# Performance work log

Measured on AMD Instinct MI355X. Metric: run time of the kernel, lower is better.

## Reference

```python
import jax, jax.numpy as jnp
import numpy as np

B, C, N, K = 2, 128, 8192, 16
EPS = 1e-5
SLOPE = 0.2


def _knn_idx(coords, k):
    # coords: [B, 3, N] -> idx: [B, N, k] (k nearest neighbors, self excluded)
    pts = jnp.transpose(coords, (0, 2, 1))            # [B, N, 3]
    sq = jnp.sum(pts * pts, axis=-1)                  # [B, N]
    d2 = sq[:, :, None] + sq[:, None, :] - 2.0 * jnp.einsum('bnd,bmd->bnm', pts, pts)
    _, idx = jax.lax.top_k(-d2, k + 1)                # nearest first; first is self (dist 0)
    return idx[:, :, 1:]


def _graph_feature(feats, idx):
    # feats: [B, C, N], idx: [B, N, k] -> [B, 2C, N, k] = concat(center, neighbor - center)
    gather = jax.vmap(lambda f, i: f[:, i])           # [C,N],[N,k] -> [C,N,k]
    neigh = gather(feats, idx)                        # [B, C, N, k]
    center = jnp.broadcast_to(feats[..., None], neigh.shape)
    return jnp.concatenate([center, neigh - center], axis=1)


def _inorm(x):
    # InstanceNorm2d, affine=False: normalize per (b, c) over spatial dims
    m = jnp.mean(x, axis=(2, 3), keepdims=True)
    v = jnp.var(x, axis=(2, 3), keepdims=True)
    return (x - m) * jax.lax.rsqrt(v + EPS)


def _block(x, W):
    # 1x1 conv (no bias) + instance norm + leaky relu
    y = jnp.einsum('oc,bcnk->bonk', W, x)
    return jax.nn.leaky_relu(_inorm(y), SLOPE)


def setup_inputs() -> dict:
    key = jax.random.key(0)
    k0, k1, k2, k3, k4 = jax.random.split(key, 5)
    coords = jax.random.normal(k0, (B, 3, N), dtype=jnp.float32)
    features = jax.random.normal(k1, (B, C, N), dtype=jnp.float32)
    W1 = jax.random.normal(k2, (C, 2 * C), dtype=jnp.float32) * 0.05
    W2 = jax.random.normal(k3, (2 * C, 2 * C), dtype=jnp.float32) * 0.05
    W3 = jax.random.normal(k4, (C, 4 * C), dtype=jnp.float32) * 0.05
    return {"coords": coords, "features": features, "W1": W1, "W2": W2, "W3": W3}


def reference(coords, features, W1, W2, W3):
    idx = _knn_idx(coords, K)                  # same coords for both gathers -> compute once
    x0 = features                              # [B, C, N]
    x1 = _block(_graph_feature(x0, idx), W1).max(axis=-1)   # [B, C, N]
    x2 = _block(_graph_feature(x1, idx), W2).max(axis=-1)   # [B, 2C, N]
    x3 = jnp.concatenate([x0, x1, x2], axis=1)              # [B, 4C, N]
    y = jnp.einsum('oc,bcn->bon', W3, x3)[..., None]        # [B, C, N, 1]
    out = jax.nn.leaky_relu(_inorm(y), SLOPE)[..., 0]       # [B, C, N]
    return out
```

## Files before the change

kernel.cpp:

```cpp
#include <hip/hip_runtime.h>
#include <math.h>

#define NB 2
#define NPTS 8192
#define CH 128
#define KNN 16
#define K17 17
#define EPSI 1e-5f
#define SLOPE 0.2f
#define NCH 32
#define CHSZ 256
#define SCAP 16
#define BIGF 3.0e38f

#define OFF_IDX   0L
#define OFF_X3    1048576L
#define OFF_UV    34603008L
#define OFF_SURV  OFF_X3
#define OFF_YM    68157440L
#define OFF_CNT   OFF_YM
#define OFF_PA    (OFF_YM + 2097152L)
#define OFF_TAU   (OFF_YM + 10485760L)
#define OFF_WM1   84934656L
#define OFF_WM2   85065728L
#define OFF_STATS 85327872L
#define OFF_PTS4  85336064L


__global__ void zero_stats_k(float* __restrict__ stats) {
  int t = blockIdx.x * 256 + threadIdx.x;
  if (t < 2048) stats[t] = 0.f;
}

__global__ void transpose_x0_k(const float* __restrict__ feat, float* __restrict__ x3) {
  __shared__ float tile[32][33];
  int b = blockIdx.z;
  int n0 = blockIdx.x * 32, c0 = blockIdx.y * 32;
  int tx = threadIdx.x;
  for (int ty = threadIdx.y; ty < 32; ty += 8)
    tile[ty][tx] = feat[((long)b * CH + c0 + ty) * NPTS + n0 + tx];
  __syncthreads();
  for (int ty = threadIdx.y; ty < 32; ty += 8)
    x3[((long)b * NPTS + n0 + ty) * 512 + c0 + tx] = tile[tx][ty];
}

__global__ void prep_w_k(const float* __restrict__ W1, const float* __restrict__ W2,
                         float* __restrict__ Wm1, float* __restrict__ Wm2) {
  int t = blockIdx.x * 256 + threadIdx.x;
  if (t < 256 * 128) {
    int r = t >> 7, k = t & 127;
    Wm1[t] = (r < 128) ? (W1[r * 256 + k] - W1[r * 256 + 128 + k])
                       : W1[(r - 128) * 256 + 128 + k];
  }
  if (t < 512 * 128) {
    int r = t >> 7, k = t & 127;
    Wm2[t] = (r < 256) ? (W2[r * 256 + k] - W2[r * 256 + 128 + k])
                       : W2[(r - 256) * 256 + 128 + k];
  }
}

__global__ void knn_prep_k(const float* __restrict__ coords, float4* __restrict__ pts) {
  int b = blockIdx.y;
  int i = blockIdx.x * 256 + threadIdx.x;
  const float* cb = coords + (long)b * 3 * NPTS;
  float x = cb[i], y = cb[NPTS + i], z = cb[2 * NPTS + i];
  float sq = __fadd_rn(__fadd_rn(__fmul_rn(x, x), __fmul_rn(y, y)), __fmul_rn(z, z));
  pts[(long)b * NPTS + i] = make_float4(x, y, z, sq);
}

#define DIST(pi, pj, d2)                                                          \
  float dot = __fadd_rn(__fadd_rn(__fmul_rn((pi).x, (pj).x), __fmul_rn((pi).y, (pj).y)), \
                        __fmul_rn((pi).z, (pj).z));                               \
  float d2 = __fsub_rn(__fadd_rn((pi).w, (pj).w), __fmul_rn(2.0f, dot));

#define KNN_INSERT(d2v, jv)                                              \
  if ((d2v) < d[K17 - 1]) {                                              \
    _Pragma("unroll")                                                    \
    for (int s = K17 - 1; s > 0; --s) {                                  \
      if ((d2v) < d[s - 1]) { d[s] = d[s - 1]; id[s] = id[s - 1]; }      \
      else if ((d2v) < d[s]) { d[s] = (d2v); id[s] = (jv); }             \
    }                                                                    \
    if ((d2v) < d[0]) { d[0] = (d2v); id[0] = (jv); }                    \
  }

__global__ __launch_bounds__(256) void knn_phaseA_k(const float4* __restrict__ pts,
                                                    float2* __restrict__ pa) {
  int b = blockIdx.y;
  int ib = blockIdx.x & 127;
  int sg = blockIdx.x >> 7;
  int i = ib * 64 + (threadIdx.x & 63);
  int sub = sg * 4 + (threadIdx.x >> 6);
  const float4* P = pts + (long)b * NPTS;
  float4 pi = P[i];
  float d0 = BIGF, d1 = BIGF;
  int i0 = 0x7fffffff, i1 = 0x7fffffff;
  int j0 = sub * 64;
  for (int jj = 0; jj < 64; ++jj) {
    float4 pj = P[j0 + jj];
    DIST(pi, pj, d2)
    if (d2 < d1) {
      if (d2 < d0) { d1 = d0; i1 = i0; d0 = d2; i0 = j0 + jj; }
      else { d1 = d2; i1 = j0 + jj; }
    }
  }
  long base = (((long)b * NPTS + i) * 32 + sub) * 2;
  pa[base] = make_float2(d0, __int_as_float(i0));
  pa[base + 1] = make_float2(d1, __int_as_float(i1));
}

__global__ __launch_bounds__(256) void knn_mergeA_k(const float2* __restrict__ pa,
                                                    float* __restrict__ tau) {
  int b = blockIdx.y;
  int i = blockIdx.x * 256 + threadIdx.x;
  float d[K17]; int id[K17];
#pragma unroll
  for (int s = 0; s < K17; ++s) { d[s] = BIGF; id[s] = 0x7fffffff; }
  long base = ((long)b * NPTS + i) * 64;
  for (int c = 0; c < 64; ++c) {
    float2 v = pa[base + c];
    if (v.x < d[K17 - 1]) {
      int j = __float_as_int(v.y);
      KNN_INSERT(v.x, j);
    }
  }
  tau[(long)b * NPTS + i] = d[K17 - 1];
}

__global__ __launch_bounds__(256) void knn_filter_k(const float4* __restrict__ pts,
                                                    const float* __restrict__ tau,
                                                    float2* __restrict__ surv,
                                                    int* __restrict__ counts) {
  int b = blockIdx.z;
  int i = blockIdx.x * 256 + threadIdx.x;
  int chunk = blockIdx.y;
  const float4* P = pts + (long)b * NPTS;
  float4 pi = P[i];
  float t = tau[(long)b * NPTS + i];
  long sbase = (((long)b * NPTS + i) * NCH + chunk) * SCAP;
  int cnt = 0;
  int j0 = chunk * CHSZ;
#pragma unroll 2
  for (int jj = 0; jj < CHSZ; ++jj) {
    float4 pj = P[j0 + jj];
    DIST(pi, pj, d2)
    if (d2 <= t) {
      if (cnt < SCAP) surv[sbase + cnt] = make_float2(d2, __int_as_float(j0 + jj));
      cnt++;
    }
  }
  counts[((long)b * NPTS + i) * NCH + chunk] = cnt;
}

__global__ __launch_bounds__(256) void knn_mergeB_k(const float2* __restrict__ surv,
                                                    const int* __restrict__ counts,
                                                    const float4* __restrict__ pts,
                                                    int* __restrict__ idxo) {
  __shared__ float2 lds[8][K17][32];
  __shared__ int ldbad[8][32];
  int b = blockIdx.y;
  int pl = threadIdx.x & 31;
  int sub = threadIdx.x >> 5;
  int i = blockIdx.x * 32 + pl;
  float d[K17]; int id[K17];
#pragma unroll
  for (int s = 0; s < K17; ++s) { d[s] = BIGF; id[s] = 0x7fffffff; }
  long cbase = ((long)b * NPTS + i) * NCH;
  int bad = 0;
  for (int c = sub * 4; c < sub * 4 + 4; ++c) {
    int cnt = counts[cbase + c];
    if (cnt > SCAP) { bad = 1; cnt = SCAP; }
    long sb = (cbase + c) * SCAP;
    for (int p = 0; p < cnt; ++p) {
      float2 v = surv[sb + p];
      if (v.x < d[K17 - 1]) {
        int j = __float_as_int(v.y);
        KNN_INSERT(v.x, j);
      }
    }
  }
  ldbad[sub][pl] = bad;
#pragma unroll
  for (int s = 0; s < K17; ++s) lds[sub][s][pl] = make_float2(d[s], __int_as_float(id[s]));
  __syncthreads();
  if ((sub & 1) == 0) {
#pragma unroll
    for (int s = 0; s < K17; ++s) {
      float2 v = lds[sub + 1][s][pl];
      if (v.x < d[K17 - 1]) {
        int j = __float_as_int(v.y);
        KNN_INSERT(v.x, j);
      }
    }
  }
  __syncthreads();
  if ((sub & 1) == 0) {
#pragma unroll
    for (int s = 0; s < K17; ++s) lds[sub >> 1][s][pl] = make_float2(d[s], __int_as_float(id[s]));
  }
  __syncthreads();
  if (sub < 2) {
#pragma unroll
    for (int s = 0; s < K17; ++s) {
      float2 v = lds[2 * sub][s][pl];
      d[s] = v.x; id[s] = __float_as_int(v.y);
    }
#pragma unroll
    for (int s = 0; s < K17; ++s) {
      float2 v = lds[2 * sub + 1][s][pl];
      if (v.x < d[K17 - 1]) {
        int j = __float_as_int(v.y);
        KNN_INSERT(v.x, j);
      }
    }
  }
  __syncthreads();
  if (sub < 2) {
#pragma unroll
    for (int s = 0; s < K17; ++s) lds[sub][s][pl] = make_float2(d[s], __int_as_float(id[s]));
  }
  __syncthreads();
  if (sub == 0) {
#pragma unroll
    for (int s = 0; s < K17; ++s) {
      float2 v = lds[0][s][pl];
      d[s] = v.x; id[s] = __float_as_int(v.y);
    }
#pragma unroll
    for (int s = 0; s < K17; ++s) {
      float2 v = lds[1][s][pl];
      if (v.x < d[K17 - 1]) {
        int j = __float_as_int(v.y);
        KNN_INSERT(v.x, j);
      }
    }
    int anybad = 0;
#pragma unroll
    for (int c = 0; c < 8; ++c) anybad |= ldbad[c][pl];
    if (anybad) {
#pragma unroll
      for (int s = 0; s < K17; ++s) { d[s] = BIGF; id[s] = 0x7fffffff; }
      const float4* P = pts + (long)b * NPTS;
      float4 pi = P[i];
      for (int j = 0; j < NPTS; ++j) {
        float4 pj = P[j];
        DIST(pi, pj, d2)
        KNN_INSERT(d2, j);
      }
    }
    long ob = ((long)b * NPTS + i) * KNN;
#pragma unroll
    for (int s = 1; s < K17; ++s) idxo[ob + s - 1] = id[s];
  }
}

#define GBN 128
#define GBM 64
#define GBK 32
__global__ __launch_bounds__(256) void gemm_xt_k(const float* __restrict__ X, int sx, long xbs,
                                                 const float* __restrict__ W, int K,
                                                 float* __restrict__ Out, int so, long obs) {
  __shared__ float Xs[GBK][GBN + 4];
  __shared__ float Ws[GBK][GBM + 4];
  int b = blockIdx.z;
  const float* Xb = X + (long)b * xbs;
  float* Ob = Out + (long)b * obs;
  int n0 = blockIdx.x * GBN, m0 = blockIdx.y * GBM;
  int tx = threadIdx.x, ty = threadIdx.y;
  int tid = ty * 16 + tx;
  float acc[8][4];
#pragma unroll
  for (int i = 0; i < 8; ++i)
#pragma unroll
    for (int j = 0; j < 4; ++j) acc[i][j] = 0.f;

  for (int k0 = 0; k0 < K; k0 += GBK) {
#pragma unroll
    for (int i = 0; i < 4; ++i) {
      int q = tid + i * 256;
      int r = q >> 3, kq = (q & 7) * 4;
      const float4 v = *(const float4*)(Xb + (long)(n0 + r) * sx + k0 + kq);
      Xs[kq][r] = v.x; Xs[kq + 1][r] = v.y; Xs[kq + 2][r] = v.z; Xs[kq + 3][r] = v.w;
    }
#pragma unroll
    for (int i = 0; i < 2; ++i) {
      int q = tid + i * 256;
      int r = q >> 3, kq = (q & 7) * 4;
      const float4 v = *(const float4*)(W + (long)(m0 + r) * K + k0 + kq);
      Ws[kq][r] = v.x; Ws[kq + 1][r] = v.y; Ws[kq + 2][r] = v.z; Ws[kq + 3][r] = v.w;
    }
    __syncthreads();
#pragma unroll
    for (int kk = 0; kk < GBK; ++kk) {
      float4 w4 = *(const float4*)&Ws[kk][tx * 4];
      float4 xa = *(const float4*)&Xs[kk][ty * 8];
      float4 xb4 = *(const float4*)&Xs[kk][ty * 8 + 4];
      float xs[8] = {xa.x, xa.y, xa.z, xa.w, xb4.x, xb4.y, xb4.z, xb4.w};
      float wv[4] = {w4.x, w4.y, w4.z, w4.w};
#pragma unroll
      for (int i = 0; i < 8; ++i)
#pragma unroll
        for (int j = 0; j < 4; ++j) acc[i][j] = fmaf(xs[i], wv[j], acc[i][j]);
    }
    __syncthreads();
  }
#pragma unroll
  for (int i = 0; i < 8; ++i) {
    float4 v = make_float4(acc[i][0], acc[i][1], acc[i][2], acc[i][3]);
    *(float4*)(Ob + (long)(n0 + ty * 8 + i) * so + m0 + tx * 4) = v;
  }
}

template <int CTILE>
__global__ __launch_bounds__(256) void edge_max_t(const float* __restrict__ uv, int S, int voff,
                                                  int Cout, const int* __restrict__ idx,
                                                  float* __restrict__ ymax,
                                                  float* __restrict__ stats) {
  constexpr int CG = CTILE / 4;
  constexpr int PSL = 256 / CG;
  __shared__ float ls[2][256][4];
  int blk = blockIdx.x;
  int c = (blk & 7) >> 1;
  int b = c >> 1;
  int ct = c & 1;
  int pblk = ((blk >> 3) << 1) | (blk & 1);
  int ch0 = ct * CTILE;
  const float* uvb = uv + (long)b * NPTS * S;
  const int* idxb = idx + (long)b * NPTS * KNN;
  float* ymb = ymax + (long)b * NPTS * Cout;
  int cg = threadIdx.x & (CG - 1);
  int ps = threadIdx.x / CG;
  int n0 = pblk * 32;
  const float* vb = uvb + voff + ch0 + 4 * cg;
  float4 s = make_float4(0.f, 0.f, 0.f, 0.f);
  float4 s2 = make_float4(0.f, 0.f, 0.f, 0.f);
  for (int p = ps; p < 32; p += PSL) {
    int n = n0 + p;
    const int* ip = idxb + n * KNN;
    int4 ia = *(const int4*)(ip);
    int4 ib4 = *(const int4*)(ip + 4);
    int4 ic = *(const int4*)(ip + 8);
    int4 id4 = *(const int4*)(ip + 12);
    int mi[KNN] = {ia.x, ia.y, ia.z, ia.w, ib4.x, ib4.y, ib4.z, ib4.w,
                   ic.x, ic.y, ic.z, ic.w, id4.x, id4.y, id4.z, id4.w};
    float4 u = *(const float4*)(uvb + (long)n * S + ch0 + 4 * cg);
    float4 mx = make_float4(-INFINITY, -INFINITY, -INFINITY, -INFINITY);
#pragma unroll
    for (int k = 0; k < KNN; ++k) {
      float4 v = *(const float4*)(vb + (long)mi[k] * S);
      float4 y;
      y.x = u.x + v.x; y.y = u.y + v.y; y.z = u.z + v.z; y.w = u.w + v.w;
      mx.x = fmaxf(mx.x, y.x); mx.y = fmaxf(mx.y, y.y);
      mx.z = fmaxf(mx.z, y.z); mx.w = fmaxf(mx.w, y.w);
      s.x += y.x; s.y += y.y; s.z += y.z; s.w += y.w;
      s2.x = fmaf(y.x, y.x, s2.x); s2.y = fmaf(y.y, y.y, s2.y);
      s2.z = fmaf(y.z, y.z, s2.z); s2.w = fmaf(y.w, y.w, s2.w);
    }
    *(float4*)(ymb + (long)n * Cout + ch0 + 4 * cg) = mx;
  }
  int t = threadIdx.x;
  ls[0][t][0] = s.x; ls[0][t][1] = s.y; ls[0][t][2] = s.z; ls[0][t][3] = s.w;
  ls[1][t][0] = s2.x; ls[1][t][1] = s2.y; ls[1][t][2] = s2.z; ls[1][t][3] = s2.w;
  __syncthreads();
  if (ps == 0) {
#pragma unroll
    for (int j = 1; j < PSL; ++j) {
      int q = j * CG + cg;
      s.x += ls[0][q][0]; s.y += ls[0][q][1]; s.z += ls[0][q][2]; s.w += ls[0][q][3];
      s2.x += ls[1][q][0]; s2.y += ls[1][q][1]; s2.z += ls[1][q][2]; s2.w += ls[1][q][3];
    }
    float* st = stats + ((long)b * Cout + ch0 + 4 * cg) * 2;
    atomicAdd(&st[0], s.x); atomicAdd(&st[1], s2.x);
    atomicAdd(&st[2], s.y); atomicAdd(&st[3], s2.y);
    atomicAdd(&st[4], s.z); atomicAdd(&st[5], s2.z);
    atomicAdd(&st[6], s.w); atomicAdd(&st[7], s2.w);
  }
}

__global__ void normalize_k(const float* __restrict__ ymax, int Cout,
                            const float* __restrict__ stats, float cinv,
                            float* __restrict__ x3, int coloff) {
  int b = blockIdx.y;
  int o = threadIdx.x & (Cout - 1);
  int n = blockIdx.x * (256 / Cout) + threadIdx.x / Cout;
  const float* st = stats + ((long)b * Cout + o) * 2;
  float mean = st[0] * cinv;
  float var = st[1] * cinv - mean * mean;
  float inv = rsqrtf(var + EPSI);
  float y = ymax[((long)b * NPTS + n) * Cout + o];
  float z = (y - mean) * inv;
  z = z >= 0.f ? z : SLOPE * z;
  x3[((long)b * NPTS + n) * 512 + coloff + o] = z;
}

__global__ void colstats_k(const float* __restrict__ y3, float* __restrict__ stats) {
  int b = blockIdx.y;
  int o = threadIdx.x & 127, slot = threadIdx.x >> 7;
  int n0 = blockIdx.x * 64;
  float s = 0.f, s2 = 0.f;
  for (int p = slot; p < 64; p += 2) {
    float y = y3[((long)b * NPTS + n0 + p) * 128 + o];
    s += y;
    s2 = fmaf(y, y, s2);
  }
  float* st = stats + ((long)b * 128 + o) * 2;
  atomicAdd(&st[0], s);
  atomicAdd(&st[1], s2);
}

__global__ void final_k(const float* __restrict__ y3, const float* __restrict__ stats,
                        float* __restrict__ out) {
  __shared__ float tile[32][33];
  int b = blockIdx.z;
  int n0 = blockIdx.x * 32, o0 = blockIdx.y * 32;
  int tx = threadIdx.x;
  for (int ty = threadIdx.y; ty < 32; ty += 8) {
    int o = o0 + tx;
    const float* st = stats + ((long)b * 128 + o) * 2;
    float mean = st[0] * (1.f / 8192.f);
    float var = st[1] * (1.f / 8192.f) - mean * mean;
    float inv = rsqrtf(var + EPSI);
    float y = y3[((long)b * NPTS + n0 + ty) * 128 + o];
    float z = (y - mean) * inv;
    tile[ty][tx] = z >= 0.f ? z : SLOPE * z;
  }
  __syncthreads();
  for (int ty = threadIdx.y; ty < 32; ty += 8)
    out[((long)b * CH + o0 + ty) * NPTS + n0 + tx] = tile[tx][ty];
}

extern "C" void kernel_launch(void* const* d_in, const int* in_sizes, int n_in,
                              void* d_out, int out_size, void* d_ws, size_t ws_size,
                              hipStream_t stream) {
  const float* coords = (const float*)d_in[0];
  const float* features = (const float*)d_in[1];
  const float* W1 = (const float*)d_in[2];
  const float* W2 = (const float*)d_in[3];
  const float* W3 = (const float*)d_in[4];
  float* out = (float*)d_out;
  char* ws = (char*)d_ws;

  int* idx = (int*)(ws + OFF_IDX);
  float* x3 = (float*)(ws + OFF_X3);
  float* uv = (float*)(ws + OFF_UV);
  float2* surv = (float2*)(ws + OFF_SURV);
  int* counts = (int*)(ws + OFF_CNT);
  float2* pa = (float2*)(ws + OFF_PA);
  float* tau = (float*)(ws + OFF_TAU);
  float* ym = (float*)(ws + OFF_YM);
  float* wm1 = (float*)(ws + OFF_WM1);
  float* wm2 = (float*)(ws + OFF_WM2);
  float* stats = (float*)(ws + OFF_STATS);
  float4* pts4 = (float4*)(ws + OFF_PTS4);

  zero_stats_k<<<8, 256, 0, stream>>>(stats);
  knn_prep_k<<<dim3(NPTS / 256, NB), 256, 0, stream>>>(coords, pts4);
  knn_phaseA_k<<<dim3(1024, NB), 256, 0, stream>>>(pts4, pa);
  knn_mergeA_k<<<dim3(NPTS / 256, NB), 256, 0, stream>>>(pa, tau);
  knn_filter_k<<<dim3(NPTS / 256, NCH, NB), 256, 0, stream>>>(pts4, tau, surv, counts);
  knn_mergeB_k<<<dim3(NPTS / 32, NB), 256, 0, stream>>>(surv, counts, pts4, idx);

  transpose_x0_k<<<dim3(NPTS / 32, CH / 32, NB), dim3(32, 8), 0, stream>>>(features, x3);
  prep_w_k<<<256, 256, 0, stream>>>(W1, W2, wm1, wm2);

  gemm_xt_k<<<dim3(NPTS / GBN, 256 / GBM, NB), dim3(16, 16), 0, stream>>>(
      x3, 512, (long)NPTS * 512, wm1, 128, uv, 256, (long)NPTS * 256);
  edge_max_t<64><<<dim3(NPTS / 32 * 2 * NB), 256, 0, stream>>>(uv, 256, 128, 128, idx, ym, stats);
  normalize_k<<<dim3(NPTS * 128 / 256, NB), 256, 0, stream>>>(ym, 128, stats,
                                                              1.0f / 131072.0f, x3, 128);
  gemm_xt_k<<<dim3(NPTS / GBN, 512 / GBM, NB), dim3(16, 16), 0, stream>>>(
      x3 + 128, 512, (long)NPTS * 512, wm2, 128, uv, 512, (long)NPTS * 512);
  edge_max_t<128><<<dim3(NPTS / 32 * 2 * NB), 256, 0, stream>>>(uv, 512, 256, 256, idx, ym,
                                                                stats + 512);
  normalize_k<<<dim3(NPTS * 256 / 256, NB), 256, 0, stream>>>(ym, 256, stats + 512,
                                                              1.0f / 131072.0f, x3, 256);
  gemm_xt_k<<<dim3(NPTS / GBN, 128 / GBM, NB), dim3(16, 16), 0, stream>>>(
      x3, 512, (long)NPTS * 512, W3, 512, ym, 128, (long)NPTS * 128);
  colstats_k<<<dim3(NPTS / 64, NB), 256, 0, stream>>>(ym, stats + 1536);
  final_k<<<dim3(NPTS / 32, CH / 32, NB), dim3(32, 8), 0, stream>>>(ym, stats + 1536, out);
}
```

Baseline: 516.1 us.

## Assign one survivor chunk per thread in kNN merge with 5-level tree reduction

The kNN merge kernel now handles 8 query points per block with 32 threads each, so each thread scans a single candidate chunk instead of 4. The per-chunk top-17 lists are combined through a generic 5-level shared-memory tree reduction, and the grid grows fourfold. This shortens the serial per-thread scan and raises parallelism, at the cost of more reduction levels and barriers and a less coalesced access pattern over the 8 points.

```diff
diff --git a/kernel.cpp b/kernel.cpp
--- a/kernel.cpp
+++ b/kernel.cpp
@@ -155,21 +155,21 @@
                                                     const int* __restrict__ counts,
                                                     const float4* __restrict__ pts,
                                                     int* __restrict__ idxo) {
-  __shared__ float2 lds[8][K17][32];
-  __shared__ int ldbad[8][32];
-  int b = blockIdx.y;
-  int pl = threadIdx.x & 31;
-  int sub = threadIdx.x >> 5;
-  int i = blockIdx.x * 32 + pl;
+  __shared__ float2 lds[16][K17][8];
+  __shared__ int ldbad[32][8];
+  int b = blockIdx.y;
+  int pl = threadIdx.x & 7;
+  int sub = threadIdx.x >> 3;
+  int i = blockIdx.x * 8 + pl;
   float d[K17]; int id[K17];
 #pragma unroll
   for (int s = 0; s < K17; ++s) { d[s] = BIGF; id[s] = 0x7fffffff; }
   long cbase = ((long)b * NPTS + i) * NCH;
-  int bad = 0;
-  for (int c = sub * 4; c < sub * 4 + 4; ++c) {
-    int cnt = counts[cbase + c];
-    if (cnt > SCAP) { bad = 1; cnt = SCAP; }
-    long sb = (cbase + c) * SCAP;
+  {
+    int cnt = counts[cbase + sub];
+    int bad = (cnt > SCAP) ? 1 : 0;
+    if (cnt > SCAP) cnt = SCAP;
+    long sb = (cbase + sub) * SCAP;
     for (int p = 0; p < cnt; ++p) {
       float2 v = surv[sb + p];
       if (v.x < d[K17 - 1]) {
@@ -177,65 +177,34 @@
         KNN_INSERT(v.x, j);
       }
     }
-  }
-  ldbad[sub][pl] = bad;
-#pragma unroll
-  for (int s = 0; s < K17; ++s) lds[sub][s][pl] = make_float2(d[s], __int_as_float(id[s]));
-  __syncthreads();
-  if ((sub & 1) == 0) {
-#pragma unroll
-    for (int s = 0; s < K17; ++s) {
-      float2 v = lds[sub + 1][s][pl];
-      if (v.x < d[K17 - 1]) {
-        int j = __float_as_int(v.y);
-        KNN_INSERT(v.x, j);
+    ldbad[sub][pl] = bad;
+  }
+#pragma unroll
+  for (int lev = 0; lev < 5; ++lev) {
+    int step = 1 << lev;
+    int mask = 2 * step - 1;
+    int slot = sub >> (lev + 1);
+    if ((sub & mask) == step) {
+#pragma unroll
+      for (int s = 0; s < K17; ++s) lds[slot][s][pl] = make_float2(d[s], __int_as_float(id[s]));
+    }
+    __syncthreads();
+    if ((sub & mask) == 0) {
+#pragma unroll
+      for (int s = 0; s < K17; ++s) {
+        float2 v = lds[slot][s][pl];
+        if (v.x < d[K17 - 1]) {
+          int j = __float_as_int(v.y);
+          KNN_INSERT(v.x, j);
+        }
       }
     }
-  }
-  __syncthreads();
-  if ((sub & 1) == 0) {
-#pragma unroll
-    for (int s = 0; s < K17; ++s) lds[sub >> 1][s][pl] = make_float2(d[s], __int_as_float(id[s]));
-  }
-  __syncthreads();
-  if (sub < 2) {
-#pragma unroll
-    for (int s = 0; s < K17; ++s) {
-      float2 v = lds[2 * sub][s][pl];
-      d[s] = v.x; id[s] = __float_as_int(v.y);
-    }
-#pragma unroll
-    for (int s = 0; s < K17; ++s) {
-      float2 v = lds[2 * sub + 1][s][pl];
-      if (v.x < d[K17 - 1]) {
-        int j = __float_as_int(v.y);
-        KNN_INSERT(v.x, j);
-      }
-    }
-  }
-  __syncthreads();
-  if (sub < 2) {
-#pragma unroll
-    for (int s = 0; s < K17; ++s) lds[sub][s][pl] = make_float2(d[s], __int_as_float(id[s]));
-  }
-  __syncthreads();
+    __syncthreads();
+  }
   if (sub == 0) {
-#pragma unroll
-    for (int s = 0; s < K17; ++s) {
-      float2 v = lds[0][s][pl];
-      d[s] = v.x; id[s] = __float_as_int(v.y);
-    }
-#pragma unroll
-    for (int s = 0; s < K17; ++s) {
-      float2 v = lds[1][s][pl];
-      if (v.x < d[K17 - 1]) {
-        int j = __float_as_int(v.y);
-        KNN_INSERT(v.x, j);
-      }
-    }
     int anybad = 0;
 #pragma unroll
-    for (int c = 0; c < 8; ++c) anybad |= ldbad[c][pl];
+    for (int c = 0; c < 32; ++c) anybad |= ldbad[c][pl];
     if (anybad) {
 #pragma unroll
       for (int s = 0; s < K17; ++s) { d[s] = BIGF; id[s] = 0x7fffffff; }
@@ -457,7 +426,7 @@
   knn_phaseA_k<<<dim3(1024, NB), 256, 0, stream>>>(pts4, pa);
   knn_mergeA_k<<<dim3(NPTS / 256, NB), 256, 0, stream>>>(pa, tau);
   knn_filter_k<<<dim3(NPTS / 256, NCH, NB), 256, 0, stream>>>(pts4, tau, surv, counts);
-  knn_mergeB_k<<<dim3(NPTS / 32, NB), 256, 0, stream>>>(surv, counts, pts4, idx);
+  knn_mergeB_k<<<dim3(NPTS / 8, NB), 256, 0, stream>>>(surv, counts, pts4, idx);
 
   transpose_x0_k<<<dim3(NPTS / 32, CH / 32, NB), dim3(32, 8), 0, stream>>>(features, x3);
   prep_w_k<<<256, 256, 0, stream>>>(W1, W2, wm1, wm2);
```

Result: slower. 698.9 us (+35.4%).
